# Optimization experiments

Measured on AMD Instinct MI355X. Metric: run time of the kernel, lower is better.

## Reference

```python
import jax, jax.numpy as jnp
import numpy as np

IMG = 128
NEAR, FAR = 1.0, 100.0
BG_EPS = 1e-3      # eps in soft_rasterize: background depth logit
SIGMA = 1e-6       # sigma_val
DIST_EPS = 1e-4    # dist_eps
GAMMA = 1e-6       # gamma_val
CHUNK = 500
B, V, F = 1, 5023, 10000


def setup_inputs():
    key = jax.random.key(0)
    k1, k2, k3, k4 = jax.random.split(key, 4)
    xy = jax.random.uniform(k1, (B, V, 2), minval=-1.0, maxval=1.0, dtype=jnp.float32)
    z = jax.random.uniform(k2, (B, V, 1), minval=5.0, maxval=15.0, dtype=jnp.float32)
    vertices = jnp.concatenate([xy, z], axis=-1)              # [B,V,3]
    faces = jax.random.randint(k3, (B, F, 3), 0, V, dtype=jnp.int32)
    attributes = jax.random.uniform(k4, (B, F, 3, 3), dtype=jnp.float32)
    return {"vertices": vertices, "faces": faces, "attributes": attributes}


def _seg_dist2(px, py, ax, ay, bx, by):
    # squared distance from pixel (px,py) to segment a-b; broadcasts [P] vs [B,C,1]
    dx = px - ax; dy = py - ay
    ex = bx - ax; ey = by - ay
    l2 = jnp.maximum(ex * ex + ey * ey, 1e-12)
    t = jnp.clip((dx * ex + dy * ey) / l2, 0.0, 1.0)
    rx = dx - t * ex; ry = dy - t * ey
    return rx * rx + ry * ry


def _render(vertices, faces, attributes):
    is_ = IMG
    P = is_ * is_
    bz = vertices.shape[0]
    v = vertices.at[..., 0].multiply(-1.0)                    # x flip (in-place in torch)
    fv = jax.vmap(lambda vv, ff: vv[ff])(v, faces)            # [B,F,3vert,3xyz]
    tex = attributes[..., :3]                                 # [B,F,3vert,3rgb]
    # fill_back=True: append copies with reversed winding
    fv = jnp.concatenate([fv, fv[:, :, ::-1, :]], axis=1)     # [B,2F,3,3]
    tex = jnp.concatenate([tex, tex[:, :, ::-1, :]], axis=1)
    F2 = fv.shape[1]
    pad = (-F2) % CHUNK
    valid = jnp.concatenate([jnp.ones((F2,), bool), jnp.zeros((pad,), bool)])
    fv = jnp.pad(fv, ((0, 0), (0, pad), (0, 0), (0, 0)))
    tex = jnp.pad(tex, ((0, 0), (0, pad), (0, 0), (0, 0)))
    n_chunks = (F2 + pad) // CHUNK
    fv = jnp.transpose(fv.reshape(bz, n_chunks, CHUNK, 3, 3), (1, 0, 2, 3, 4))
    tex = jnp.transpose(tex.reshape(bz, n_chunks, CHUNK, 3, 3), (1, 0, 2, 3, 4))
    valid = valid.reshape(n_chunks, CHUNK)

    # pixel centers in [-1,1]; row 0 is the top of the image (y flipped as in CUDA)
    xs = (2.0 * jnp.arange(is_, dtype=jnp.float32) + 1.0 - is_) / is_
    ys = (2.0 * (is_ - 1 - jnp.arange(is_, dtype=jnp.float32)) + 1.0 - is_) / is_
    px = jnp.broadcast_to(xs[None, :], (is_, is_)).reshape(-1)  # [P]
    py = jnp.broadcast_to(ys[:, None], (is_, is_)).reshape(-1)

    thr = DIST_EPS * SIGMA
    inv_g = 1.0 / GAMMA

    def step(carry, inp):
        m, s, cacc, prod = carry                # [B,P],[B,P],[B,3,P],[B,P]
        fvc, txc, vld = inp                     # [B,C,3,3],[B,C,3,3],[C]
        x0 = fvc[:, :, 0, 0][..., None]; y0 = fvc[:, :, 0, 1][..., None]; z0 = fvc[:, :, 0, 2][..., None]
        x1 = fvc[:, :, 1, 0][..., None]; y1 = fvc[:, :, 1, 1][..., None]; z1 = fvc[:, :, 1, 2][..., None]
        x2 = fvc[:, :, 2, 0][..., None]; y2 = fvc[:, :, 2, 1][..., None]; z2 = fvc[:, :, 2, 2][..., None]
        det = (y1 - y2) * (x0 - x2) + (x2 - x1) * (y0 - y2)   # [B,C,1]
        det = jnp.where(jnp.abs(det) < 1e-10, jnp.where(det < 0, -1e-10, 1e-10), det)
        w0 = ((y1 - y2) * (px - x2) + (x2 - x1) * (py - y2)) / det  # [B,C,P]
        w1 = ((y2 - y0) * (px - x2) + (x0 - x2) * (py - y2)) / det
        w2 = 1.0 - w0 - w1
        inside = (w0 >= 0) & (w1 >= 0) & (w2 >= 0)
        dis = jnp.minimum(jnp.minimum(_seg_dist2(px, py, x0, y0, x1, y1),
                                      _seg_dist2(px, py, x1, y1, x2, y2)),
                          _seg_dist2(px, py, x2, y2, x0, y0))     # [B,C,P] squared dist
        contrib = (inside | (dis < thr)) & vld[None, :, None]
        sgn = jnp.where(inside, 1.0, -1.0)
        Dp = jnp.where(contrib, jax.nn.sigmoid(sgn * dis / SIGMA), 0.0)
        prod = prod * jnp.prod(1.0 - Dp, axis=1)                  # alpha: prod(1-D)
        # clipped barycentric + perspective-correct depth
        c0 = jnp.clip(w0, 0.0, 1.0); c1 = jnp.clip(w1, 0.0, 1.0); c2 = jnp.clip(w2, 0.0, 1.0)
        csum = jnp.maximum(c0 + c1 + c2, 1e-5)
        c0 = c0 / csum; c1 = c1 / csum; c2 = c2 / csum
        zp_inv = c0 / z0 + c1 / z1 + c2 / z2
        zp = 1.0 / jnp.where(jnp.abs(zp_inv) < 1e-12, 1e-12, zp_inv)
        front = (y2 - y0) * (x1 - x0) < (y1 - y0) * (x2 - x0)     # [B,C,1]
        rgb_m = contrib & front & (zp >= NEAR) & (zp <= FAR)
        zpn = (FAR - zp) / (FAR - NEAR)
        new_m = jnp.maximum(m, jnp.max(jnp.where(rgb_m, zpn, -jnp.inf), axis=1))
        e = jnp.exp(jnp.where(rgb_m, (zpn - new_m[:, None, :]) * inv_g, -jnp.inf)) * Dp
        scale = jnp.exp((m - new_m) * inv_g)                      # [B,P]
        wc = jnp.stack([c0, c1, c2], axis=2)                      # [B,C,3,P]
        col = jnp.einsum('bcvp,bcvk->bckp', wc, txc)              # interpolated rgb
        s = s * scale + jnp.sum(e, axis=1)
        cacc = cacc * scale[:, None, :] + jnp.sum(e[:, :, None, :] * col, axis=1)
        return (new_m, s, cacc, prod), None

    m0 = jnp.full((bz, P), BG_EPS, jnp.float32)   # background logit = eps
    s0 = jnp.ones((bz, P), jnp.float32)           # exp((eps - m0)/gamma) = 1
    c0_ = jnp.zeros((bz, 3, P), jnp.float32)      # black background
    p0 = jnp.ones((bz, P), jnp.float32)
    (m, s, cacc, prod), _ = jax.lax.scan(jax.checkpoint(step), (m0, s0, c0_, p0), (fv, tex, valid))
    rgb = cacc / s[:, None, :]
    alpha = 1.0 - prod
    return jnp.concatenate([rgb, alpha[:, None, :]], axis=1).reshape(bz, 4, is_, is_)


def reference(vertices, faces, attributes):
    return _render(vertices, faces, attributes)
```

## Files before the change

### kernel.cpp

```cpp
#include <hip/hip_runtime.h>
#include <math.h>


#define NFACE 10000
#define IMG   128
#define P_TOT (IMG*IMG)
#define FSTR  40
#define NTILE 64
#define NQ    4
#define CAPQ  2500
#define CAP   (CAPQ*NQ)
#define BMAX  4096
#define NB    1024
#define CH    256
#define NCH   40
#define Z_LO  0.85f
#define Z_W   (0.12f/1024.0f)

__device__ __forceinline__ float rcp_nr(float x) {
    float r = __builtin_amdgcn_rcpf(x);
    r = r * __builtin_fmaf(-x, r, 2.0f);
    return r;
}

__device__ __forceinline__ float segd(float px, float py, float ax, float ay,
                                      float bx, float by, float il) {
    float dx = px - ax, dy = py - ay;
    float ex = bx - ax, ey = by - ay;
    float t = (dx * ex + dy * ey) * il;
    t = fminf(fmaxf(t, 0.0f), 1.0f);
    float rx = dx - t * ex, ry = dy - t * ey;
    return rx * rx + ry * ry;
}

__device__ __forceinline__ float rfl_f(float x) {
    return __uint_as_float(__builtin_amdgcn_readfirstlane(__float_as_uint(x)));
}

__device__ __forceinline__ int zbucket(float zub) {
    int b = (int)((zub - Z_LO) * (1.0f / Z_W));
    return min(max(b, 0), NB - 1);
}

__global__ __launch_bounds__(256) void k_prehist(const float* __restrict__ v,
                                                 const int* __restrict__ fc,
                                                 const float* __restrict__ at,
                                                 float* __restrict__ fb,
                                                 int* __restrict__ hist) {
    __shared__ int lh[NB];
    int c = blockIdx.x, tid = threadIdx.x;
    for (int j = tid; j < NB; j += 256) lh[j] = 0;
    __syncthreads();

    int f = c * CH + tid;
    if (f < NFACE) {
        int i0 = fc[3 * f], i1 = fc[3 * f + 1], i2 = fc[3 * f + 2];
        float x0 = -v[3 * i0], y0 = v[3 * i0 + 1], z0 = v[3 * i0 + 2];
        float x1 = -v[3 * i1], y1 = v[3 * i1 + 1], z1 = v[3 * i1 + 2];
        float x2 = -v[3 * i2], y2 = v[3 * i2 + 1], z2 = v[3 * i2 + 2];

        float det = (y1 - y2) * (x0 - x2) + (x2 - x1) * (y0 - y2);
        if (fabsf(det) < 1e-10f) det = (det < 0.0f) ? -1e-10f : 1e-10f;
        float a0 = y1 - y2, b0 = x2 - x1, a1 = y2 - y0, b1 = x0 - x2, detp = det;
        if (det < 0.0f) { detp = -det; a0 = -a0; b0 = -b0; a1 = -a1; b1 = -b1; }

        float a2 = a0 + a1, b2 = b0 + b1;
        float g0 = fmaxf(sqrtf(a0 * a0 + b0 * b0), 1e-12f);
        float g1 = fmaxf(sqrtf(a1 * a1 + b1 * b1), 1e-12f);
        float g2 = fmaxf(sqrtf(a2 * a2 + b2 * b2), 1e-12f);
        const float MARG = 3e-5f, AG = 1e-9f;
        float m0 = -(MARG * g0 + AG), m1 = -(MARG * g1 + AG), m2 = -(MARG * g2 + AG);

        float e01x = x1 - x0, e01y = y1 - y0;
        float e12x = x2 - x1, e12y = y2 - y1;
        float e20x = x0 - x2, e20y = y0 - y2;
        float il01 = 1.0f / fmaxf(e01x * e01x + e01y * e01y, 1e-12f);
        float il12 = 1.0f / fmaxf(e12x * e12x + e12y * e12y, 1e-12f);
        float il20 = 1.0f / fmaxf(e20x * e20x + e20y * e20y, 1e-12f);

        const float BM = 2e-5f;
        float bxmin = fminf(fminf(x0, x1), x2) - BM, bxmax = fmaxf(fmaxf(x0, x1), x2) + BM;
        float bymin = fminf(fminf(y0, y1), y2) - BM, bymax = fmaxf(fmaxf(y0, y1), y2) + BM;

        int mult = (((y2 - y0) * (x1 - x0)) < ((y1 - y0) * (x2 - x0)))
                 + (((y0 - y2) * (x1 - x2)) < ((y1 - y2) * (x0 - x2)));

        float zmin = fminf(fminf(z0, z1), z2);
        float zub = (100.0f - zmin) / 99.0f + 2e-6f;

        float* F = fb + (size_t)f * FSTR;
        F[0] = bxmin; F[1] = bxmax; F[2] = bymin; F[3] = bymax;
        F[4] = x2; F[5] = y2; F[6] = a0; F[7] = b0;
        F[8] = a1; F[9] = b1; F[10] = detp; F[11] = zub;
        F[12] = m0; F[13] = m1; F[14] = m2; F[15] = (float)mult;
        F[16] = x0; F[17] = y0; F[18] = x1; F[19] = y1;
        F[20] = il01; F[21] = il12; F[22] = il20; F[23] = 1.0f / detp;
        F[24] = 1.0f / z0; F[25] = 1.0f / z1; F[26] = 1.0f / z2;
        F[27] = 1.0f / g0; F[28] = 1.0f / g1; F[29] = 1.0f / g2;
#pragma unroll
        for (int k = 0; k < 9; k++) F[30 + k] = at[(size_t)f * 9 + k];
        F[39] = 0.0f;

        atomicAdd(&lh[zbucket(zub)], 1);
    }
    __syncthreads();
    for (int j = tid; j < NB; j += 256) hist[c * NB + j] = lh[j];
}

__global__ __launch_bounds__(1024) void k_scan(int* __restrict__ hist) {
    __shared__ int a[NB];
    int t = threadIdx.x;
    int tot = 0;
    for (int c = 0; c < NCH; c++) tot += hist[c * NB + t];
    a[t] = tot;
    for (int off = 1; off < NB; off <<= 1) {
        __syncthreads();
        int v = a[t] + ((t + off < NB) ? a[t + off] : 0);
        __syncthreads();
        a[t] = v;
    }
    int r = a[t] - tot;
    for (int c = 0; c < NCH; c++) {
        int h = hist[c * NB + t];
        hist[c * NB + t] = r;
        r += h;
    }
}

__global__ __launch_bounds__(256) void k_scatterre(const float* __restrict__ fb,
                                                   const int* __restrict__ hist,
                                                   float* __restrict__ fb2) {
    __shared__ int sb[CH];
    int c = blockIdx.x, tid = threadIdx.x;
    int f = c * CH + tid;
    bool valid = (f < NFACE);
    int b = valid ? zbucket(fb[(size_t)f * FSTR + 11]) : -1;
    sb[tid] = b;
    __syncthreads();
    if (valid) {
        int rank = 0;
        for (int j = 0; j < CH; j++) {
            int v2 = sb[j];
            rank += (j < tid && v2 == b) ? 1 : 0;
        }
        int pos = hist[c * NB + b] + rank;
        const float4* src = (const float4*)(fb + (size_t)f * FSTR);
        float4* dst = (float4*)(fb2 + (size_t)pos * FSTR);
#pragma unroll
        for (int k = 0; k < 10; k++) dst[k] = src[k];
        fb2[(size_t)pos * FSTR + 11] = Z_LO + (float)(b + 1) * Z_W + 1e-7f;
    }
}

__global__ __launch_bounds__(256) void k_bin(const float* __restrict__ fb2,
                                             float2* __restrict__ tmeta,
                                             int* __restrict__ cnt4) {
    int t = blockIdx.x >> 2, q = blockIdx.x & 3;
    int tid = threadIdx.x, wv = tid >> 6, lane = tid & 63;
    int tx = t & 7, ty = t >> 3;
    float x_lo = (float)(2 * (tx * 16) + 1 - IMG) / (float)IMG;
    float x_hi = (float)(2 * (tx * 16 + 15) + 1 - IMG) / (float)IMG;
    float y_hi = (float)(127 - 2 * (ty * 16)) / (float)IMG;
    float y_lo = (float)(127 - 2 * (ty * 16 + 15)) / (float)IMG;
    float cx = 0.5f * (x_lo + x_hi), hx = 0.5f * (x_hi - x_lo);
    float cy = 0.5f * (y_lo + y_hi), hy = 0.5f * (y_hi - y_lo);

    __shared__ int wc[4];
    int cnt = 0;
    int f0 = q * CAPQ;
    for (int base = f0; base < f0 + CAPQ; base += 256) {
        int j = base + tid;
        bool ov = false;
        float zub = 0.0f;
        if (j < f0 + CAPQ) {
            const float4* H = (const float4*)(fb2 + (size_t)j * FSTR);
            float4 h0 = H[0], h1 = H[1], h2 = H[2], h3 = H[3];
            ov = (h0.x <= x_hi) & (h0.y >= x_lo) & (h0.z <= y_hi) & (h0.w >= y_lo);
            if (ov) {
                float dx = cx - h1.x, dy = cy - h1.y;
                float mx0 = h1.z * dx + h1.w * dy + fabsf(h1.z) * hx + fabsf(h1.w) * hy;
                float mx1 = h2.x * dx + h2.y * dy + fabsf(h2.x) * hx + fabsf(h2.y) * hy;
                float A2 = -(h1.z + h2.x), B2 = -(h1.w + h2.y);
                float mx2 = h2.z + A2 * dx + B2 * dy + fabsf(A2) * hx + fabsf(B2) * hy;
                ov = (mx0 >= h3.x) & (mx1 >= h3.y) & (mx2 >= h3.z);
                zub = h2.w;
            }
        }
        unsigned long long mask = __ballot(ov);
        if (lane == 0) wc[wv] = __popcll(mask);
        __syncthreads();
        int off = cnt;
        for (int w = 0; w < 4; ++w) {
            if (w < wv) off += wc[w];
        }
        if (ov) {
            int pos = off + __popcll(mask & ((1ull << lane) - 1ull));
            tmeta[(size_t)t * CAP + q * CAPQ + pos] =
                make_float2(zub, __int_as_float(j));
        }
        cnt += wc[0] + wc[1] + wc[2] + wc[3];
        __syncthreads();
    }
    if (tid == 0) cnt4[t * 4 + q] = cnt;
}

__global__ __launch_bounds__(64) void k_map(const int* __restrict__ cnt4,
                                            int* __restrict__ map,
                                            int* __restrict__ starts,
                                            int* __restrict__ segs,
                                            int B) {
    int lane = threadIdx.x;
    int len = cnt4[4 * lane] + cnt4[4 * lane + 1] + cnt4[4 * lane + 2] + cnt4[4 * lane + 3];
    int tot = len;
    for (int o = 32; o > 0; o >>= 1) tot += __shfl_down(tot, o);
    tot = __shfl(tot, 0);
    int St = max(1, (int)(((long long)len * (long long)(B - NTILE)) /
                          (long long)max(tot, 1)));
    __shared__ int sS[64], sP[64];
    sS[lane] = St;
    __syncthreads();
    if (lane == 0) {
        int acc = 0;
        for (int t = 0; t < 64; ++t) { sP[t] = acc; acc += sS[t]; }
    }
    __syncthreads();
    for (int i = lane; i < B; i += 64) map[i] = -1;
    __syncthreads();
    int st = sP[lane];
    starts[lane] = st;
    segs[lane] = St;
    for (int s = 0; s < St; ++s) map[st + s] = (lane << 16) | s;
}

__global__ __launch_bounds__(256) void k_main(const float* __restrict__ fb2,
                                              const float2* __restrict__ tmeta,
                                              const int* __restrict__ cnt4,
                                              const int* __restrict__ map,
                                              const int* __restrict__ segs,
                                              float* __restrict__ part) {
    int bid = blockIdx.x;
    int mv = map[bid];
    if (mv < 0) return;
    int t = mv >> 16, seg = mv & 0xffff;
    int S = segs[t];

    int tid = threadIdx.x;
    int tx = t & 7, ty = t >> 3;
    int col = tx * 16 + (tid & 15);
    int row = ty * 16 + (tid >> 4);
    float px = (float)(2 * col + 1 - IMG) / (float)IMG;
    float py = (float)(2 * (IMG - 1 - row) + 1 - IMG) / (float)IMG;

    const float2* pm = tmeta + (size_t)t * CAP;

    float m = -__builtin_inff();
    float s = 0.0f, ca = 0.0f, cb = 0.0f, cc = 0.0f, pr = 1.0f;

    const float NEAR_T = 4.3e-3f;
    const float ZM = 1.3e-4f;

    bool done = false;
    for (int q = 0; q < 4 && !done; ++q) {
        int qlen = cnt4[t * 4 + q];
        for (int i = seg; i < qlen; i += S) {
            float2 mt = pm[q * CAPQ + i];
            float zcur = rfl_f(mt.x);
            if (__all((pr == 0.0f) & (zcur <= m - ZM))) { done = true; break; }
            int fj = __builtin_amdgcn_readfirstlane(__float_as_int(mt.y));
            const float4* H = (const float4*)(fb2 + (size_t)fj * FSTR);
            float4 g0 = H[0], g1 = H[1], g2 = H[2], g3 = H[3];

            bool inbox = (px >= g0.x) & (px <= g0.y) & (py >= g0.z) & (py <= g0.w);
            if (!__any(inbox)) continue;

            float x2 = g1.x, y2 = g1.y;
            float dx2 = px - x2, dy2 = py - y2;
            float num0 = g1.z * dx2 + g1.w * dy2;
            float num1 = g2.x * dx2 + g2.y * dy2;
            float detp = g2.z;
            float num2 = detp - num0 - num1;
            bool maybe = inbox & (num0 >= g3.x) & (num1 >= g3.y) & (num2 >= g3.z);
            if (!__any(maybe)) continue;

            const float* F = fb2 + (size_t)fj * FSTR;

            bool inside = (num0 >= 0.0f) & (num1 >= 0.0f) & (num2 >= 0.0f);
            bool inside_l = inside & inbox;

            float lin0 = num0 * F[27];
            float lin1 = num1 * F[28];
            float lin2 = num2 * F[29];
            float lbmin = fminf(fminf(lin0, lin1), lin2);

            bool outNear = maybe & (!inside);
            bool nearIn  = inside_l & (lbmin < NEAR_T);
            bool anyNear = __any(nearIn | outNear);

            float dis = 1e9f;
            float Dp;
            if (anyNear) {
                bool needAll = __any(outNear);
                float x0 = F[16], y0 = F[17], x1 = F[18], y1 = F[19];
                float d01 = 1e9f, d12 = 1e9f, d20 = 1e9f;
                if (needAll | __any(inside_l & (lin2 < NEAR_T)))
                    d01 = segd(px, py, x0, y0, x1, y1, F[20]);
                if (needAll | __any(inside_l & (lin0 < NEAR_T)))
                    d12 = segd(px, py, x1, y1, x2, y2, F[21]);
                if (needAll | __any(inside_l & (lin1 < NEAR_T)))
                    d20 = segd(px, py, x2, y2, x0, y0, F[22]);
                dis = fminf(fminf(d01, d12), d20);

                float qq = dis * 1e6f;
                float xs_ = inside ? qq : -qq;
                float tt = __expf(-fabsf(xs_));
                float Dpn = (xs_ >= 0.0f ? 1.0f : tt) * rcp_nr(1.0f + tt);
                bool nearl = nearIn | outNear;
                Dp = nearl ? Dpn : (inside_l ? 1.0f : 0.0f);
            } else {
                Dp = inside_l ? 1.0f : 0.0f;
            }

            bool contrib = inside_l | (outNear & (dis < 1e-10f));
            Dp = contrib ? Dp : 0.0f;
            float omd = 1.0f - Dp;
            pr *= contrib ? (omd * omd) : 1.0f;

            float multf = g3.w;
            bool doz = contrib & (multf > 0.0f);
            if (__any(doz & (zcur > m - ZM))) {
                float rdetp = F[23];
                float w0 = num0 * rdetp;
                float w1 = num1 * rdetp;
                float c0 = fminf(fmaxf(w0, 0.0f), 1.0f);
                float c1 = fminf(fmaxf(w1, 0.0f), 1.0f);
                float c2 = fminf(fmaxf(1.0f - w0 - w1, 0.0f), 1.0f);
                float csum = fmaxf(c0 + c1 + c2, 1e-5f);
                float rcs = rcp_nr(csum);
                c0 *= rcs; c1 *= rcs; c2 *= rcs;
                float zpi = c0 * F[24] + c1 * F[25] + c2 * F[26];
                if (fabsf(zpi) < 1e-12f) zpi = 1e-12f;
                float zp = rcp_nr(zpi);
                if (doz & (zp >= 1.0f) & (zp <= 100.0f)) {
                    float zpn = (100.0f - zp) / 99.0f;
                    if (zpn > m) {
                        float scl = __expf((m - zpn) * 1e6f);
                        s *= scl; ca *= scl; cb *= scl; cc *= scl;
                        m = zpn;
                    }
                    float arg = (zpn - m) * 1e6f;
                    if (arg > -110.0f) {
                        float e = __expf(arg) * Dp * multf;
                        float col0 = c0 * F[30] + c1 * F[33] + c2 * F[36];
                        float col1 = c0 * F[31] + c1 * F[34] + c2 * F[37];
                        float col2 = c0 * F[32] + c1 * F[35] + c2 * F[38];
                        s += e; ca += e * col0; cb += e * col1; cc += e * col2;
                    }
                }
            }
        }
    }

    size_t pb = (size_t)bid * 6 * 256;
    part[pb + 0 * 256 + tid] = m;
    part[pb + 1 * 256 + tid] = s;
    part[pb + 2 * 256 + tid] = ca;
    part[pb + 3 * 256 + tid] = cb;
    part[pb + 4 * 256 + tid] = cc;
    part[pb + 5 * 256 + tid] = pr;
}

__global__ __launch_bounds__(1024) void k_reduce(const float* __restrict__ part,
                                                 const int* __restrict__ starts,
                                                 const int* __restrict__ segs,
                                                 float* __restrict__ out) {
    __shared__ float sm[4][256], ss[4][256], sa[4][256], sb2[4][256],
                     sc[4][256], sp[4][256];
    int t = blockIdx.x;
    int tid = threadIdx.x;
    int q = tid & 255, sub = tid >> 8;
    int start = starts[t], S = segs[t];

    const float NINF = -__builtin_inff();
    float mp = NINF;
    for (int sgi = sub; sgi < S; sgi += 4)
        mp = fmaxf(mp, part[((size_t)(start + sgi) * 6 + 0) * 256 + q]);
    float sum = 0.0f, a = 0.0f, b = 0.0f, c = 0.0f, pr = 1.0f;
    for (int sgi = sub; sgi < S; sgi += 4) {
        const float* r = part + ((size_t)(start + sgi) * 6) * 256;
        float rm = r[0 * 256 + q];
        float w = (rm == NINF) ? 0.0f : __expf((rm - mp) * 1e6f);
        pr *= r[5 * 256 + q];
        if (__any(w != 0.0f)) {
            sum += r[1 * 256 + q] * w;
            a += r[2 * 256 + q] * w;
            b += r[3 * 256 + q] * w;
            c += r[4 * 256 + q] * w;
        }
    }
    sm[sub][q] = mp; ss[sub][q] = sum; sa[sub][q] = a;
    sb2[sub][q] = b; sc[sub][q] = c;  sp[sub][q] = pr;
    __syncthreads();
    if (sub == 0) {
        int tx = t & 7, ty = t >> 3;
        int col = tx * 16 + (q & 15);
        int row = ty * 16 + (q >> 4);
        int p = row * IMG + col;
        float M = 0.001f;
#pragma unroll
        for (int k = 0; k < 4; k++) M = fmaxf(M, sm[k][q]);
        float SUM = __expf((0.001f - M) * 1e6f);
        float A = 0.0f, B2 = 0.0f, C = 0.0f, PR = 1.0f;
#pragma unroll
        for (int k = 0; k < 4; k++) {
            float w = __expf((sm[k][q] - M) * 1e6f);
            SUM += ss[k][q] * w;
            A += sa[k][q] * w;
            B2 += sb2[k][q] * w;
            C += sc[k][q] * w;
            PR *= sp[k][q];
        }
        out[0 * P_TOT + p] = A / SUM;
        out[1 * P_TOT + p] = B2 / SUM;
        out[2 * P_TOT + p] = C / SUM;
        out[3 * P_TOT + p] = 1.0f - PR;
    }
}

extern "C" void kernel_launch(void* const* d_in, const int* in_sizes, int n_in,
                              void* d_out, int out_size, void* d_ws, size_t ws_size,
                              hipStream_t stream) {
    const float* verts = (const float*)d_in[0];
    const int*   faces = (const int*)d_in[1];
    const float* attrs = (const float*)d_in[2];
    float* out = (float*)d_out;
    float* ws  = (float*)d_ws;

    float*  fb    = ws;
    int*    hist  = (int*)(fb + (size_t)NFACE * FSTR);
    float*  fb2   = (float*)(hist + NCH * NB);
    float2* tmeta = (float2*)(fb2 + (size_t)NFACE * FSTR);
    int*    cnt4  = (int*)(tmeta + (size_t)NTILE * CAP);
    int*    map   = cnt4 + NTILE * 4;
    int*    starts= map + BMAX;
    int*    segs  = starts + NTILE;
    float*  part  = (float*)(segs + NTILE);

    size_t used_f = 2 * (size_t)NFACE * FSTR + NCH * NB
                  + 2 * (size_t)NTILE * CAP + NTILE * 4 + BMAX + 2 * NTILE;
    long   rem_f  = (long)(ws_size / 4) - (long)used_f;
    int B = (int)(rem_f / (6 * 256));
    if (B > BMAX) B = BMAX;
    if (B < 256)  B = 256;

    k_prehist<<<NCH, 256, 0, stream>>>(verts, faces, attrs, fb, hist);
    k_scan<<<1, 1024, 0, stream>>>(hist);
    k_scatterre<<<NCH, 256, 0, stream>>>(fb, hist, fb2);
    k_bin<<<NTILE * NQ, 256, 0, stream>>>(fb2, tmeta, cnt4);
    k_map<<<1, 64, 0, stream>>>(cnt4, map, starts, segs, B);
    k_main<<<B, 256, 0, stream>>>(fb2, tmeta, cnt4, map, segs, part);
    k_reduce<<<NTILE, 1024, 0, stream>>>(part, starts, segs, out);
}
```

Before: 139.1 us.

## Bin faces into 8x8 pixel regions and assign one wavefront per region segment

Replaces the 64 tiles of 16x16 pixels with 256 regions of 8x8 pixels. Each binning block now tests faces against four sub-regions and writes plain face-index lists, so the main kernel reads the depth bound from the face record instead of a separate (z, index) list. The main kernel now maps work per wavefront (64 lanes = one 8x8 region) rather than per 256-thread block, with a binary-search work map over up to 16K slots. The aim is tighter face culling per wave and less divergent wasted work, at the cost of more binning passes, more partials and extra barriers in k_bin.

```diff
diff --git a/kernel.cpp b/kernel.cpp
--- a/kernel.cpp
+++ b/kernel.cpp
@@ -6,11 +6,10 @@
 #define IMG   128
 #define P_TOT (IMG*IMG)
 #define FSTR  40
-#define NTILE 64
+#define NREG  256
 #define NQ    4
 #define CAPQ  2500
-#define CAP   (CAPQ*NQ)
-#define BMAX  4096
+#define WMAX  16384
 #define NB    1024
 #define CH    256
 #define NCH   40
@@ -31,10 +30,6 @@
     t = fminf(fmaxf(t, 0.0f), 1.0f);
     float rx = dx - t * ex, ry = dy - t * ey;
     return rx * rx + ry * ry;
-}
-
-__device__ __forceinline__ float rfl_f(float x) {
-    return __uint_as_float(__builtin_amdgcn_readfirstlane(__float_as_uint(x)));
 }
 
 __device__ __forceinline__ int zbucket(float zub) {
@@ -107,9 +102,11 @@
     for (int j = tid; j < NB; j += 256) hist[c * NB + j] = lh[j];
 }
 
-__global__ __launch_bounds__(1024) void k_scan(int* __restrict__ hist) {
+__global__ __launch_bounds__(1024) void k_scan(int* __restrict__ hist,
+                                               int* __restrict__ len) {
     __shared__ int a[NB];
     int t = threadIdx.x;
+    if (t < NREG) len[t] = 0;
     int tot = 0;
     for (int c = 0; c < NCH; c++) tot += hist[c * NB + t];
     a[t] = tot;
@@ -153,106 +150,145 @@
 }
 
 __global__ __launch_bounds__(256) void k_bin(const float* __restrict__ fb2,
-                                             float2* __restrict__ tmeta,
-                                             int* __restrict__ cnt4) {
+                                             int* __restrict__ rlist,
+                                             int* __restrict__ cnt16,
+                                             int* __restrict__ len) {
     int t = blockIdx.x >> 2, q = blockIdx.x & 3;
     int tid = threadIdx.x, wv = tid >> 6, lane = tid & 63;
     int tx = t & 7, ty = t >> 3;
-    float x_lo = (float)(2 * (tx * 16) + 1 - IMG) / (float)IMG;
-    float x_hi = (float)(2 * (tx * 16 + 15) + 1 - IMG) / (float)IMG;
-    float y_hi = (float)(127 - 2 * (ty * 16)) / (float)IMG;
-    float y_lo = (float)(127 - 2 * (ty * 16 + 15)) / (float)IMG;
-    float cx = 0.5f * (x_lo + x_hi), hx = 0.5f * (x_hi - x_lo);
-    float cy = 0.5f * (y_lo + y_hi), hy = 0.5f * (y_hi - y_lo);
+
+    float rxlo[4], rxhi[4], rylo[4], ryhi[4], rcx[4], rcy[4], rhx[4], rhy[4];
+    int rgl[4];
+#pragma unroll
+    for (int rl = 0; rl < 4; rl++) {
+        int sx = rl & 1, sy = rl >> 1;
+        int rx = tx * 2 + sx, ry = ty * 2 + sy;
+        rgl[rl] = ry * 16 + rx;
+        float xl = (float)(2 * (rx * 8) + 1 - IMG) / (float)IMG;
+        float xh = (float)(2 * (rx * 8 + 7) + 1 - IMG) / (float)IMG;
+        float yh = (float)(127 - 2 * (ry * 8)) / (float)IMG;
+        float yl = (float)(127 - 2 * (ry * 8 + 7)) / (float)IMG;
+        rxlo[rl] = xl; rxhi[rl] = xh; rylo[rl] = yl; ryhi[rl] = yh;
+        rcx[rl] = 0.5f * (xl + xh); rhx[rl] = 0.5f * (xh - xl);
+        rcy[rl] = 0.5f * (yl + yh); rhy[rl] = 0.5f * (yh - yl);
+    }
+    float tx_lo = rxlo[0], tx_hi = rxhi[1];
+    float ty_lo = rylo[2], ty_hi = ryhi[0];
 
     __shared__ int wc[4];
-    int cnt = 0;
+    int cnt[4] = {0, 0, 0, 0};
     int f0 = q * CAPQ;
     for (int base = f0; base < f0 + CAPQ; base += 256) {
         int j = base + tid;
-        bool ov = false;
-        float zub = 0.0f;
-        if (j < f0 + CAPQ) {
+        bool ov[4] = {false, false, false, false};
+        {
             const float4* H = (const float4*)(fb2 + (size_t)j * FSTR);
             float4 h0 = H[0], h1 = H[1], h2 = H[2], h3 = H[3];
-            ov = (h0.x <= x_hi) & (h0.y >= x_lo) & (h0.z <= y_hi) & (h0.w >= y_lo);
-            if (ov) {
-                float dx = cx - h1.x, dy = cy - h1.y;
-                float mx0 = h1.z * dx + h1.w * dy + fabsf(h1.z) * hx + fabsf(h1.w) * hy;
-                float mx1 = h2.x * dx + h2.y * dy + fabsf(h2.x) * hx + fabsf(h2.y) * hy;
+            bool tov = (h0.x <= tx_hi) & (h0.y >= tx_lo) & (h0.z <= ty_hi) & (h0.w >= ty_lo);
+            if (tov) {
                 float A2 = -(h1.z + h2.x), B2 = -(h1.w + h2.y);
-                float mx2 = h2.z + A2 * dx + B2 * dy + fabsf(A2) * hx + fabsf(B2) * hy;
-                ov = (mx0 >= h3.x) & (mx1 >= h3.y) & (mx2 >= h3.z);
-                zub = h2.w;
+#pragma unroll
+                for (int rl = 0; rl < 4; rl++) {
+                    bool o = (h0.x <= rxhi[rl]) & (h0.y >= rxlo[rl]) &
+                             (h0.z <= ryhi[rl]) & (h0.w >= rylo[rl]);
+                    if (o) {
+                        float dx = rcx[rl] - h1.x, dy = rcy[rl] - h1.y;
+                        float hx = rhx[rl], hy = rhy[rl];
+                        float mx0 = h1.z * dx + h1.w * dy + fabsf(h1.z) * hx + fabsf(h1.w) * hy;
+                        float mx1 = h2.x * dx + h2.y * dy + fabsf(h2.x) * hx + fabsf(h2.y) * hy;
+                        float mx2 = h2.z + A2 * dx + B2 * dy + fabsf(A2) * hx + fabsf(B2) * hy;
+                        o = (mx0 >= h3.x) & (mx1 >= h3.y) & (mx2 >= h3.z);
+                    }
+                    ov[rl] = o;
+                }
             }
         }
-        unsigned long long mask = __ballot(ov);
-        if (lane == 0) wc[wv] = __popcll(mask);
-        __syncthreads();
-        int off = cnt;
-        for (int w = 0; w < 4; ++w) {
-            if (w < wv) off += wc[w];
-        }
-        if (ov) {
-            int pos = off + __popcll(mask & ((1ull << lane) - 1ull));
-            tmeta[(size_t)t * CAP + q * CAPQ + pos] =
-                make_float2(zub, __int_as_float(j));
-        }
-        cnt += wc[0] + wc[1] + wc[2] + wc[3];
-        __syncthreads();
-    }
-    if (tid == 0) cnt4[t * 4 + q] = cnt;
-}
-
-__global__ __launch_bounds__(64) void k_map(const int* __restrict__ cnt4,
-                                            int* __restrict__ map,
-                                            int* __restrict__ starts,
-                                            int* __restrict__ segs,
-                                            int B) {
-    int lane = threadIdx.x;
-    int len = cnt4[4 * lane] + cnt4[4 * lane + 1] + cnt4[4 * lane + 2] + cnt4[4 * lane + 3];
-    int tot = len;
-    for (int o = 32; o > 0; o >>= 1) tot += __shfl_down(tot, o);
-    tot = __shfl(tot, 0);
-    int St = max(1, (int)(((long long)len * (long long)(B - NTILE)) /
-                          (long long)max(tot, 1)));
-    __shared__ int sS[64], sP[64];
-    sS[lane] = St;
-    __syncthreads();
-    if (lane == 0) {
+#pragma unroll
+        for (int rl = 0; rl < 4; rl++) {
+            unsigned long long mask = __ballot(ov[rl]);
+            if (lane == 0) wc[wv] = __popcll(mask);
+            __syncthreads();
+            int off = cnt[rl];
+            for (int w = 0; w < 4; ++w) {
+                if (w < wv) off += wc[w];
+            }
+            if (ov[rl]) {
+                int pos = off + __popcll(mask & ((1ull << lane) - 1ull));
+                rlist[((size_t)rgl[rl] * 4 + q) * CAPQ + pos] = j;
+            }
+            cnt[rl] += wc[0] + wc[1] + wc[2] + wc[3];
+            __syncthreads();
+        }
+    }
+    if (tid == 0) {
+#pragma unroll
+        for (int rl = 0; rl < 4; rl++) {
+            cnt16[rgl[rl] * 4 + q] = cnt[rl];
+            atomicAdd(&len[rgl[rl]], cnt[rl]);
+        }
+    }
+}
+
+__global__ __launch_bounds__(256) void k_map(const int* __restrict__ len,
+                                             int* __restrict__ map,
+                                             int* __restrict__ starts,
+                                             int* __restrict__ Sarr,
+                                             int W) {
+    __shared__ int sL[NREG], sS[NREG], sP[NREG], sTot;
+    int rr = threadIdx.x;
+    sL[rr] = len[rr];
+    __syncthreads();
+    if (rr == 0) {
+        int tot = 0;
+        for (int k = 0; k < NREG; k++) tot += sL[k];
+        sTot = max(tot, 1);
+    }
+    __syncthreads();
+    int tot = sTot;
+    int S = max(1, (int)(((long long)sL[rr] * (long long)(W - NREG)) /
+                         (long long)tot));
+    sS[rr] = S;
+    __syncthreads();
+    if (rr == 0) {
         int acc = 0;
-        for (int t = 0; t < 64; ++t) { sP[t] = acc; acc += sS[t]; }
-    }
-    __syncthreads();
-    for (int i = lane; i < B; i += 64) map[i] = -1;
-    __syncthreads();
-    int st = sP[lane];
-    starts[lane] = st;
-    segs[lane] = St;
-    for (int s = 0; s < St; ++s) map[st + s] = (lane << 16) | s;
+        for (int k = 0; k < NREG; k++) { sP[k] = acc; acc += sS[k]; }
+    }
+    __syncthreads();
+    starts[rr] = sP[rr];
+    Sarr[rr] = sS[rr];
+    int used = sP[NREG - 1] + sS[NREG - 1];
+    for (int i = rr; i < W; i += 256) {
+        int mv = -1;
+        if (i < used) {
+            int lo = 0, hi = NREG - 1;
+            while (lo < hi) {
+                int mid = (lo + hi + 1) >> 1;
+                if (sP[mid] <= i) lo = mid; else hi = mid - 1;
+            }
+            mv = (lo << 16) | (i - sP[lo]);
+        }
+        map[i] = mv;
+    }
 }
 
 __global__ __launch_bounds__(256) void k_main(const float* __restrict__ fb2,
-                                              const float2* __restrict__ tmeta,
-                                              const int* __restrict__ cnt4,
+                                              const int* __restrict__ rlist,
+                                              const int* __restrict__ cnt16,
                                               const int* __restrict__ map,
-                                              const int* __restrict__ segs,
+                                              const int* __restrict__ Sarr,
                                               float* __restrict__ part) {
-    int bid = blockIdx.x;
-    int mv = map[bid];
+    int slot = blockIdx.x * 4 + (threadIdx.x >> 6);
+    int lane = threadIdx.x & 63;
+    int mv = map[slot];
     if (mv < 0) return;
-    int t = mv >> 16, seg = mv & 0xffff;
-    int S = segs[t];
-
-    int tid = threadIdx.x;
-    int tx = t & 7, ty = t >> 3;
-    int col = tx * 16 + (tid & 15);
-    int row = ty * 16 + (tid >> 4);
+    int r = mv >> 16, seg = mv & 0xffff;
+    int Sr = Sarr[r];
+    int rx = r & 15, ry = r >> 4;
+    int col = rx * 8 + (lane & 7);
+    int row = ry * 8 + (lane >> 3);
     float px = (float)(2 * col + 1 - IMG) / (float)IMG;
     float py = (float)(2 * (IMG - 1 - row) + 1 - IMG) / (float)IMG;
 
-    const float2* pm = tmeta + (size_t)t * CAP;
-
     float m = -__builtin_inff();
     float s = 0.0f, ca = 0.0f, cb = 0.0f, cc = 0.0f, pr = 1.0f;
 
@@ -261,14 +297,14 @@
 
     bool done = false;
     for (int q = 0; q < 4 && !done; ++q) {
-        int qlen = cnt4[t * 4 + q];
-        for (int i = seg; i < qlen; i += S) {
-            float2 mt = pm[q * CAPQ + i];
-            float zcur = rfl_f(mt.x);
-            if (__all((pr == 0.0f) & (zcur <= m - ZM))) { done = true; break; }
-            int fj = __builtin_amdgcn_readfirstlane(__float_as_int(mt.y));
+        int qlen = cnt16[r * 4 + q];
+        const int* lst = rlist + ((size_t)r * 4 + q) * CAPQ;
+        for (int i = seg; i < qlen; i += Sr) {
+            int fj = __builtin_amdgcn_readfirstlane(lst[i]);
             const float4* H = (const float4*)(fb2 + (size_t)fj * FSTR);
             float4 g0 = H[0], g1 = H[1], g2 = H[2], g3 = H[3];
+            float zcur = g2.w;
+            if (__all((pr == 0.0f) & (zcur <= m - ZM))) { done = true; break; }
 
             bool inbox = (px >= g0.x) & (px <= g0.y) & (py >= g0.z) & (py <= g0.w);
             if (!__any(inbox)) continue;
@@ -360,64 +396,64 @@
         }
     }
 
-    size_t pb = (size_t)bid * 6 * 256;
-    part[pb + 0 * 256 + tid] = m;
-    part[pb + 1 * 256 + tid] = s;
-    part[pb + 2 * 256 + tid] = ca;
-    part[pb + 3 * 256 + tid] = cb;
-    part[pb + 4 * 256 + tid] = cc;
-    part[pb + 5 * 256 + tid] = pr;
-}
-
-__global__ __launch_bounds__(1024) void k_reduce(const float* __restrict__ part,
-                                                 const int* __restrict__ starts,
-                                                 const int* __restrict__ segs,
-                                                 float* __restrict__ out) {
-    __shared__ float sm[4][256], ss[4][256], sa[4][256], sb2[4][256],
-                     sc[4][256], sp[4][256];
-    int t = blockIdx.x;
+    size_t pb = (size_t)slot * 6 * 64;
+    part[pb + 0 * 64 + lane] = m;
+    part[pb + 1 * 64 + lane] = s;
+    part[pb + 2 * 64 + lane] = ca;
+    part[pb + 3 * 64 + lane] = cb;
+    part[pb + 4 * 64 + lane] = cc;
+    part[pb + 5 * 64 + lane] = pr;
+}
+
+__global__ __launch_bounds__(256) void k_reduce(const float* __restrict__ part,
+                                                const int* __restrict__ starts,
+                                                const int* __restrict__ Sarr,
+                                                float* __restrict__ out) {
+    __shared__ float sm[4][64], ss[4][64], sa[4][64], sb2[4][64],
+                     sc[4][64], sp[4][64];
+    int r = blockIdx.x;
     int tid = threadIdx.x;
-    int q = tid & 255, sub = tid >> 8;
-    int start = starts[t], S = segs[t];
+    int lane = tid & 63, sub = tid >> 6;
+    int start = starts[r], S = Sarr[r];
 
     const float NINF = -__builtin_inff();
     float mp = NINF;
     for (int sgi = sub; sgi < S; sgi += 4)
-        mp = fmaxf(mp, part[((size_t)(start + sgi) * 6 + 0) * 256 + q]);
+        mp = fmaxf(mp, part[((size_t)(start + sgi) * 6 + 0) * 64 + lane]);
     float sum = 0.0f, a = 0.0f, b = 0.0f, c = 0.0f, pr = 1.0f;
     for (int sgi = sub; sgi < S; sgi += 4) {
-        const float* r = part + ((size_t)(start + sgi) * 6) * 256;
-        float rm = r[0 * 256 + q];
+        const float* rp = part + ((size_t)(start + sgi) * 6) * 64;
+        float rm = rp[0 * 64 + lane];
         float w = (rm == NINF) ? 0.0f : __expf((rm - mp) * 1e6f);
-        pr *= r[5 * 256 + q];
+        pr *= rp[5 * 64 + lane];
         if (__any(w != 0.0f)) {
-            sum += r[1 * 256 + q] * w;
-            a += r[2 * 256 + q] * w;
-            b += r[3 * 256 + q] * w;
-            c += r[4 * 256 + q] * w;
-        }
-    }
-    sm[sub][q] = mp; ss[sub][q] = sum; sa[sub][q] = a;
-    sb2[sub][q] = b; sc[sub][q] = c;  sp[sub][q] = pr;
+            sum += rp[1 * 64 + lane] * w;
+            a += rp[2 * 64 + lane] * w;
+            b += rp[3 * 64 + lane] * w;
+            c += rp[4 * 64 + lane] * w;
+        }
+    }
+    sm[sub][lane] = mp; ss[sub][lane] = sum; sa[sub][lane] = a;
+    sb2[sub][lane] = b; sc[sub][lane] = c;  sp[sub][lane] = pr;
     __syncthreads();
     if (sub == 0) {
-        int tx = t & 7, ty = t >> 3;
-        int col = tx * 16 + (q & 15);
-        int row = ty * 16 + (q >> 4);
+        int rx = r & 15, ry = r >> 4;
+        int col = rx * 8 + (lane & 7);
+        int row = ry * 8 + (lane >> 3);
         int p = row * IMG + col;
         float M = 0.001f;
 #pragma unroll
-        for (int k = 0; k < 4; k++) M = fmaxf(M, sm[k][q]);
+        for (int k = 0; k < 4; k++) M = fmaxf(M, sm[k][lane]);
         float SUM = __expf((0.001f - M) * 1e6f);
         float A = 0.0f, B2 = 0.0f, C = 0.0f, PR = 1.0f;
 #pragma unroll
         for (int k = 0; k < 4; k++) {
-            float w = __expf((sm[k][q] - M) * 1e6f);
-            SUM += ss[k][q] * w;
-            A += sa[k][q] * w;
-            B2 += sb2[k][q] * w;
-            C += sc[k][q] * w;
-            PR *= sp[k][q];
+            float w = __expf((sm[k][lane] - M) * 1e6f);
+            SUM += ss[k][lane] * w;
+            A += sa[k][lane] * w;
+            B2 += sb2[k][lane] * w;
+            C += sc[k][lane] * w;
+            PR *= sp[k][lane];
         }
         out[0 * P_TOT + p] = A / SUM;
         out[1 * P_TOT + p] = B2 / SUM;
@@ -435,28 +471,31 @@
     float* out = (float*)d_out;
     float* ws  = (float*)d_ws;
 
-    float*  fb    = ws;
-    int*    hist  = (int*)(fb + (size_t)NFACE * FSTR);
-    float*  fb2   = (float*)(hist + NCH * NB);
-    float2* tmeta = (float2*)(fb2 + (size_t)NFACE * FSTR);
-    int*    cnt4  = (int*)(tmeta + (size_t)NTILE * CAP);
-    int*    map   = cnt4 + NTILE * 4;
-    int*    starts= map + BMAX;
-    int*    segs  = starts + NTILE;
-    float*  part  = (float*)(segs + NTILE);
+    float* fb     = ws;
+    int*   hist   = (int*)(fb + (size_t)NFACE * FSTR);
+    float* fb2    = (float*)(hist + NCH * NB);
+    int*   rlist  = (int*)(fb2 + (size_t)NFACE * FSTR);
+    int*   cnt16  = rlist + (size_t)NREG * 4 * CAPQ;
+    int*   len    = cnt16 + NREG * 4;
+    int*   map    = len + NREG;
+    int*   starts = map + WMAX;
+    int*   Sarr   = starts + NREG;
+    float* part   = (float*)(Sarr + NREG);
 
     size_t used_f = 2 * (size_t)NFACE * FSTR + NCH * NB
-                  + 2 * (size_t)NTILE * CAP + NTILE * 4 + BMAX + 2 * NTILE;
+                  + (size_t)NREG * 4 * CAPQ + NREG * 4 + NREG + WMAX + 2 * NREG;
     long   rem_f  = (long)(ws_size / 4) - (long)used_f;
-    int B = (int)(rem_f / (6 * 256));
-    if (B > BMAX) B = BMAX;
-    if (B < 256)  B = 256;
+    int W = (int)(rem_f / (6 * 64));
+    if (W > WMAX) W = WMAX;
+    if (W < 1024) W = 1024;
+    W &= ~3;
+    int B = W / 4;
 
     k_prehist<<<NCH, 256, 0, stream>>>(verts, faces, attrs, fb, hist);
-    k_scan<<<1, 1024, 0, stream>>>(hist);
+    k_scan<<<1, 1024, 0, stream>>>(hist, len);
     k_scatterre<<<NCH, 256, 0, stream>>>(fb, hist, fb2);
-    k_bin<<<NTILE * NQ, 256, 0, stream>>>(fb2, tmeta, cnt4);
-    k_map<<<1, 64, 0, stream>>>(cnt4, map, starts, segs, B);
-    k_main<<<B, 256, 0, stream>>>(fb2, tmeta, cnt4, map, segs, part);
-    k_reduce<<<NTILE, 1024, 0, stream>>>(part, starts, segs, out);
-}
+    k_bin<<<NREG, 256, 0, stream>>>(fb2, rlist, cnt16, len);
+    k_map<<<1, 256, 0, stream>>>(len, map, starts, Sarr, W);
+    k_main<<<B, 256, 0, stream>>>(fb2, rlist, cnt16, map, Sarr, part);
+    k_reduce<<<NREG, 256, 0, stream>>>(part, starts, Sarr, out);
+}
```

Measured after the change: 173.8 us. +24.9%, slower.

## Drop k_map launch by deriving tile-segment map in-kernel; transpose histogram layout

Applied to the files above, without the earlier changes.

Removes the separate k_map launch: k_main and k_reduce now each recompute the per-tile segment counts and prefix offsets from cnt4 in shared memory, and k_main finds its tile with a binary search. The per-chunk histogram is transposed to bucket-major so the scan kernel reads each row contiguously, and the face chunk size is halved, giving 79 blocks of 128 threads instead of 40 of 256 for more parallelism in the preprocessing kernels. The aim is to cut one launch and some serialized small-kernel latency, at the cost of redundant map derivation (a serial 64-iteration loop on thread 0) in every k_main block.

```diff
diff --git a/kernel.cpp b/kernel.cpp
--- a/kernel.cpp
+++ b/kernel.cpp
@@ -12,8 +12,8 @@
 #define CAP   (CAPQ*NQ)
 #define BMAX  4096
 #define NB    1024
-#define CH    256
-#define NCH   40
+#define CH    128
+#define NCH   79
 #define Z_LO  0.85f
 #define Z_W   (0.12f/1024.0f)
 
@@ -42,14 +42,14 @@
     return min(max(b, 0), NB - 1);
 }
 
-__global__ __launch_bounds__(256) void k_prehist(const float* __restrict__ v,
+__global__ __launch_bounds__(128) void k_prehist(const float* __restrict__ v,
                                                  const int* __restrict__ fc,
                                                  const float* __restrict__ at,
                                                  float* __restrict__ fb,
                                                  int* __restrict__ hist) {
     __shared__ int lh[NB];
     int c = blockIdx.x, tid = threadIdx.x;
-    for (int j = tid; j < NB; j += 256) lh[j] = 0;
+    for (int j = tid; j < NB; j += 128) lh[j] = 0;
     __syncthreads();
 
     int f = c * CH + tid;
@@ -104,14 +104,16 @@
         atomicAdd(&lh[zbucket(zub)], 1);
     }
     __syncthreads();
-    for (int j = tid; j < NB; j += 256) hist[c * NB + j] = lh[j];
+    for (int j = tid; j < NB; j += 128) hist[j * NCH + c] = lh[j];
 }
 
 __global__ __launch_bounds__(1024) void k_scan(int* __restrict__ hist) {
     __shared__ int a[NB];
     int t = threadIdx.x;
+    int* row = hist + t * NCH;
     int tot = 0;
-    for (int c = 0; c < NCH; c++) tot += hist[c * NB + t];
+#pragma unroll 8
+    for (int c = 0; c < NCH; c++) tot += row[c];
     a[t] = tot;
     for (int off = 1; off < NB; off <<= 1) {
         __syncthreads();
@@ -120,14 +122,15 @@
         a[t] = v;
     }
     int r = a[t] - tot;
+#pragma unroll 8
     for (int c = 0; c < NCH; c++) {
-        int h = hist[c * NB + t];
-        hist[c * NB + t] = r;
+        int h = row[c];
+        row[c] = r;
         r += h;
     }
 }
 
-__global__ __launch_bounds__(256) void k_scatterre(const float* __restrict__ fb,
+__global__ __launch_bounds__(128) void k_scatterre(const float* __restrict__ fb,
                                                    const int* __restrict__ hist,
                                                    float* __restrict__ fb2) {
     __shared__ int sb[CH];
@@ -143,7 +146,7 @@
             int v2 = sb[j];
             rank += (j < tid && v2 == b) ? 1 : 0;
         }
-        int pos = hist[c * NB + b] + rank;
+        int pos = hist[b * NCH + c] + rank;
         const float4* src = (const float4*)(fb + (size_t)f * FSTR);
         float4* dst = (float4*)(fb2 + (size_t)pos * FSTR);
 #pragma unroll
@@ -204,47 +207,47 @@
     if (tid == 0) cnt4[t * 4 + q] = cnt;
 }
 
-__global__ __launch_bounds__(64) void k_map(const int* __restrict__ cnt4,
-                                            int* __restrict__ map,
-                                            int* __restrict__ starts,
-                                            int* __restrict__ segs,
-                                            int B) {
-    int lane = threadIdx.x;
-    int len = cnt4[4 * lane] + cnt4[4 * lane + 1] + cnt4[4 * lane + 2] + cnt4[4 * lane + 3];
-    int tot = len;
-    for (int o = 32; o > 0; o >>= 1) tot += __shfl_down(tot, o);
-    tot = __shfl(tot, 0);
-    int St = max(1, (int)(((long long)len * (long long)(B - NTILE)) /
-                          (long long)max(tot, 1)));
-    __shared__ int sS[64], sP[64];
-    sS[lane] = St;
-    __syncthreads();
-    if (lane == 0) {
+__device__ __forceinline__ void derive_map(const int* __restrict__ cnt4,
+                                           int B, int tid,
+                                           int* sLen, int* sS, int* sP,
+                                           int* sUsed) {
+    if (tid < NTILE)
+        sLen[tid] = cnt4[4 * tid] + cnt4[4 * tid + 1]
+                  + cnt4[4 * tid + 2] + cnt4[4 * tid + 3];
+    __syncthreads();
+    if (tid == 0) {
+        int tot = 0;
+        for (int k = 0; k < NTILE; k++) tot += sLen[k];
+        tot = max(tot, 1);
         int acc = 0;
-        for (int t = 0; t < 64; ++t) { sP[t] = acc; acc += sS[t]; }
-    }
-    __syncthreads();
-    for (int i = lane; i < B; i += 64) map[i] = -1;
-    __syncthreads();
-    int st = sP[lane];
-    starts[lane] = st;
-    segs[lane] = St;
-    for (int s = 0; s < St; ++s) map[st + s] = (lane << 16) | s;
+        for (int k = 0; k < NTILE; k++) {
+            int S = max(1, (int)(((long long)sLen[k] * (long long)(B - NTILE)) /
+                                 (long long)tot));
+            sS[k] = S; sP[k] = acc; acc += S;
+        }
+        *sUsed = acc;
+    }
+    __syncthreads();
 }
 
 __global__ __launch_bounds__(256) void k_main(const float* __restrict__ fb2,
                                               const float2* __restrict__ tmeta,
                                               const int* __restrict__ cnt4,
-                                              const int* __restrict__ map,
-                                              const int* __restrict__ segs,
-                                              float* __restrict__ part) {
+                                              float* __restrict__ part,
+                                              int B) {
+    __shared__ int sLen[NTILE], sS[NTILE], sP[NTILE], sUsed;
+    int tid = threadIdx.x;
+    derive_map(cnt4, B, tid, sLen, sS, sP, &sUsed);
     int bid = blockIdx.x;
-    int mv = map[bid];
-    if (mv < 0) return;
-    int t = mv >> 16, seg = mv & 0xffff;
-    int S = segs[t];
-
-    int tid = threadIdx.x;
+    if (bid >= sUsed) return;
+    int lo = 0, hi = NTILE - 1;
+    while (lo < hi) {
+        int mid = (lo + hi + 1) >> 1;
+        if (sP[mid] <= bid) lo = mid; else hi = mid - 1;
+    }
+    int t = lo, seg = bid - sP[lo];
+    int S = sS[t];
+
     int tx = t & 7, ty = t >> 3;
     int col = tx * 16 + (tid & 15);
     int row = ty * 16 + (tid >> 4);
@@ -262,8 +265,9 @@
     bool done = false;
     for (int q = 0; q < 4 && !done; ++q) {
         int qlen = cnt4[t * 4 + q];
+        const float2* pq = pm + q * CAPQ;
         for (int i = seg; i < qlen; i += S) {
-            float2 mt = pm[q * CAPQ + i];
+            float2 mt = pq[i];
             float zcur = rfl_f(mt.x);
             if (__all((pr == 0.0f) & (zcur <= m - ZM))) { done = true; break; }
             int fj = __builtin_amdgcn_readfirstlane(__float_as_int(mt.y));
@@ -370,15 +374,18 @@
 }
 
 __global__ __launch_bounds__(1024) void k_reduce(const float* __restrict__ part,
-                                                 const int* __restrict__ starts,
-                                                 const int* __restrict__ segs,
-                                                 float* __restrict__ out) {
+                                                 const int* __restrict__ cnt4,
+                                                 float* __restrict__ out,
+                                                 int B) {
+    __shared__ int sLen[NTILE], sS[NTILE], sP[NTILE], sUsed;
     __shared__ float sm[4][256], ss[4][256], sa[4][256], sb2[4][256],
                      sc[4][256], sp[4][256];
     int t = blockIdx.x;
     int tid = threadIdx.x;
+    derive_map(cnt4, B, tid, sLen, sS, sP, &sUsed);
+    int start = sP[t], S = sS[t];
+
     int q = tid & 255, sub = tid >> 8;
-    int start = starts[t], S = segs[t];
 
     const float NINF = -__builtin_inff();
     float mp = NINF;
@@ -437,26 +444,22 @@
 
     float*  fb    = ws;
     int*    hist  = (int*)(fb + (size_t)NFACE * FSTR);
-    float*  fb2   = (float*)(hist + NCH * NB);
+    float*  fb2   = (float*)(hist + NB * NCH);
     float2* tmeta = (float2*)(fb2 + (size_t)NFACE * FSTR);
     int*    cnt4  = (int*)(tmeta + (size_t)NTILE * CAP);
-    int*    map   = cnt4 + NTILE * 4;
-    int*    starts= map + BMAX;
-    int*    segs  = starts + NTILE;
-    float*  part  = (float*)(segs + NTILE);
-
-    size_t used_f = 2 * (size_t)NFACE * FSTR + NCH * NB
-                  + 2 * (size_t)NTILE * CAP + NTILE * 4 + BMAX + 2 * NTILE;
+    float*  part  = (float*)(cnt4 + NTILE * 4);
+
+    size_t used_f = 2 * (size_t)NFACE * FSTR + NB * NCH
+                  + 2 * (size_t)NTILE * CAP + NTILE * 4;
     long   rem_f  = (long)(ws_size / 4) - (long)used_f;
     int B = (int)(rem_f / (6 * 256));
     if (B > BMAX) B = BMAX;
     if (B < 256)  B = 256;
 
-    k_prehist<<<NCH, 256, 0, stream>>>(verts, faces, attrs, fb, hist);
+    k_prehist<<<NCH, 128, 0, stream>>>(verts, faces, attrs, fb, hist);
     k_scan<<<1, 1024, 0, stream>>>(hist);
-    k_scatterre<<<NCH, 256, 0, stream>>>(fb, hist, fb2);
+    k_scatterre<<<NCH, 128, 0, stream>>>(fb, hist, fb2);
     k_bin<<<NTILE * NQ, 256, 0, stream>>>(fb2, tmeta, cnt4);
-    k_map<<<1, 64, 0, stream>>>(cnt4, map, starts, segs, B);
-    k_main<<<B, 256, 0, stream>>>(fb2, tmeta, cnt4, map, segs, part);
-    k_reduce<<<NTILE, 1024, 0, stream>>>(part, starts, segs, out);
-}
+    k_main<<<B, 256, 0, stream>>>(fb2, tmeta, cnt4, part, B);
+    k_reduce<<<NTILE, 1024, 0, stream>>>(part, cnt4, out, B);
+}
```

New measurement: 198.5 us. 1.43x slower.

## Batch-stage face headers into shared memory cooperatively per block

Applied to the files above, without the earlier changes.

The per-face inner loop is restructured to process faces in batches of sixteen. Threads cooperatively load each batch's face metadata and 64-byte header into LDS between block barriers, replacing per-wave dependent global loads for every face. The aim is to hide global load latency by issuing sixteen faces' loads in parallel. The cost is two block syncs plus a sync-count per batch, and early termination now needs all four waves to agree before the block stops iterating.

```diff
diff --git a/kernel.cpp b/kernel.cpp
--- a/kernel.cpp
+++ b/kernel.cpp
@@ -16,6 +16,7 @@
 #define NCH   40
 #define Z_LO  0.85f
 #define Z_W   (0.12f/1024.0f)
+#define BATCH 16
 
 __device__ __forceinline__ float rcp_nr(float x) {
     float r = __builtin_amdgcn_rcpf(x);
@@ -238,6 +239,10 @@
                                               const int* __restrict__ map,
                                               const int* __restrict__ segs,
                                               float* __restrict__ part) {
+    __shared__ float  sz[BATCH];
+    __shared__ int    sf[BATCH];
+    __shared__ float4 sh[BATCH][4];
+
     int bid = blockIdx.x;
     int mv = map[bid];
     if (mv < 0) return;
@@ -259,101 +264,127 @@
     const float NEAR_T = 4.3e-3f;
     const float ZM = 1.3e-4f;
 
-    bool done = false;
-    for (int q = 0; q < 4 && !done; ++q) {
+    bool mydone = false;
+    bool alldone = false;
+
+    for (int q = 0; q < 4 && !alldone; ++q) {
         int qlen = cnt4[t * 4 + q];
-        for (int i = seg; i < qlen; i += S) {
-            float2 mt = pm[q * CAPQ + i];
-            float zcur = rfl_f(mt.x);
-            if (__all((pr == 0.0f) & (zcur <= m - ZM))) { done = true; break; }
-            int fj = __builtin_amdgcn_readfirstlane(__float_as_int(mt.y));
-            const float4* H = (const float4*)(fb2 + (size_t)fj * FSTR);
-            float4 g0 = H[0], g1 = H[1], g2 = H[2], g3 = H[3];
-
-            bool inbox = (px >= g0.x) & (px <= g0.y) & (py >= g0.z) & (py <= g0.w);
-            if (!__any(inbox)) continue;
-
-            float x2 = g1.x, y2 = g1.y;
-            float dx2 = px - x2, dy2 = py - y2;
-            float num0 = g1.z * dx2 + g1.w * dy2;
-            float num1 = g2.x * dx2 + g2.y * dy2;
-            float detp = g2.z;
-            float num2 = detp - num0 - num1;
-            bool maybe = inbox & (num0 >= g3.x) & (num1 >= g3.y) & (num2 >= g3.z);
-            if (!__any(maybe)) continue;
-
-            const float* F = fb2 + (size_t)fj * FSTR;
-
-            bool inside = (num0 >= 0.0f) & (num1 >= 0.0f) & (num2 >= 0.0f);
-            bool inside_l = inside & inbox;
-
-            float lin0 = num0 * F[27];
-            float lin1 = num1 * F[28];
-            float lin2 = num2 * F[29];
-            float lbmin = fminf(fminf(lin0, lin1), lin2);
-
-            bool outNear = maybe & (!inside);
-            bool nearIn  = inside_l & (lbmin < NEAR_T);
-            bool anyNear = __any(nearIn | outNear);
-
-            float dis = 1e9f;
-            float Dp;
-            if (anyNear) {
-                bool needAll = __any(outNear);
-                float x0 = F[16], y0 = F[17], x1 = F[18], y1 = F[19];
-                float d01 = 1e9f, d12 = 1e9f, d20 = 1e9f;
-                if (needAll | __any(inside_l & (lin2 < NEAR_T)))
-                    d01 = segd(px, py, x0, y0, x1, y1, F[20]);
-                if (needAll | __any(inside_l & (lin0 < NEAR_T)))
-                    d12 = segd(px, py, x1, y1, x2, y2, F[21]);
-                if (needAll | __any(inside_l & (lin1 < NEAR_T)))
-                    d20 = segd(px, py, x2, y2, x0, y0, F[22]);
-                dis = fminf(fminf(d01, d12), d20);
-
-                float qq = dis * 1e6f;
-                float xs_ = inside ? qq : -qq;
-                float tt = __expf(-fabsf(xs_));
-                float Dpn = (xs_ >= 0.0f ? 1.0f : tt) * rcp_nr(1.0f + tt);
-                bool nearl = nearIn | outNear;
-                Dp = nearl ? Dpn : (inside_l ? 1.0f : 0.0f);
-            } else {
-                Dp = inside_l ? 1.0f : 0.0f;
+        const float2* pq = pm + q * CAPQ;
+        for (int ib = seg; ib < qlen; ib += BATCH * S) {
+            int ndone = __syncthreads_count((int)mydone);
+            if (ndone == 256) { alldone = true; break; }
+            if (tid < BATCH) {
+                int e = ib + tid * S;
+                if (e < qlen) {
+                    float2 mt = pq[e];
+                    sz[tid] = mt.x;
+                    sf[tid] = __float_as_int(mt.y);
+                } else {
+                    sf[tid] = -1;
+                }
             }
-
-            bool contrib = inside_l | (outNear & (dis < 1e-10f));
-            Dp = contrib ? Dp : 0.0f;
-            float omd = 1.0f - Dp;
-            pr *= contrib ? (omd * omd) : 1.0f;
-
-            float multf = g3.w;
-            bool doz = contrib & (multf > 0.0f);
-            if (__any(doz & (zcur > m - ZM))) {
-                float rdetp = F[23];
-                float w0 = num0 * rdetp;
-                float w1 = num1 * rdetp;
-                float c0 = fminf(fmaxf(w0, 0.0f), 1.0f);
-                float c1 = fminf(fmaxf(w1, 0.0f), 1.0f);
-                float c2 = fminf(fmaxf(1.0f - w0 - w1, 0.0f), 1.0f);
-                float csum = fmaxf(c0 + c1 + c2, 1e-5f);
-                float rcs = rcp_nr(csum);
-                c0 *= rcs; c1 *= rcs; c2 *= rcs;
-                float zpi = c0 * F[24] + c1 * F[25] + c2 * F[26];
-                if (fabsf(zpi) < 1e-12f) zpi = 1e-12f;
-                float zp = rcp_nr(zpi);
-                if (doz & (zp >= 1.0f) & (zp <= 100.0f)) {
-                    float zpn = (100.0f - zp) / 99.0f;
-                    if (zpn > m) {
-                        float scl = __expf((m - zpn) * 1e6f);
-                        s *= scl; ca *= scl; cb *= scl; cc *= scl;
-                        m = zpn;
+            __syncthreads();
+            if (tid < BATCH * 4) {
+                int k = tid >> 2, j = tid & 3;
+                int fj = sf[k];
+                if (fj >= 0)
+                    sh[k][j] = ((const float4*)(fb2 + (size_t)fj * FSTR))[j];
+            }
+            __syncthreads();
+            if (!mydone) {
+                for (int k = 0; k < BATCH; ++k) {
+                    int fj = __builtin_amdgcn_readfirstlane(sf[k]);
+                    if (fj < 0) break;
+                    float zcur = sz[k];
+                    if (__all((pr == 0.0f) & (zcur <= m - ZM))) { mydone = true; break; }
+                    float4 g0 = sh[k][0], g1 = sh[k][1], g2 = sh[k][2], g3 = sh[k][3];
+
+                    bool inbox = (px >= g0.x) & (px <= g0.y) & (py >= g0.z) & (py <= g0.w);
+                    if (!__any(inbox)) continue;
+
+                    float x2 = g1.x, y2 = g1.y;
+                    float dx2 = px - x2, dy2 = py - y2;
+                    float num0 = g1.z * dx2 + g1.w * dy2;
+                    float num1 = g2.x * dx2 + g2.y * dy2;
+                    float detp = g2.z;
+                    float num2 = detp - num0 - num1;
+                    bool maybe = inbox & (num0 >= g3.x) & (num1 >= g3.y) & (num2 >= g3.z);
+                    if (!__any(maybe)) continue;
+
+                    const float* F = fb2 + (size_t)fj * FSTR;
+
+                    bool inside = (num0 >= 0.0f) & (num1 >= 0.0f) & (num2 >= 0.0f);
+                    bool inside_l = inside & inbox;
+
+                    float lin0 = num0 * F[27];
+                    float lin1 = num1 * F[28];
+                    float lin2 = num2 * F[29];
+                    float lbmin = fminf(fminf(lin0, lin1), lin2);
+
+                    bool outNear = maybe & (!inside);
+                    bool nearIn  = inside_l & (lbmin < NEAR_T);
+                    bool anyNear = __any(nearIn | outNear);
+
+                    float dis = 1e9f;
+                    float Dp;
+                    if (anyNear) {
+                        bool needAll = __any(outNear);
+                        float x0 = F[16], y0 = F[17], x1 = F[18], y1 = F[19];
+                        float d01 = 1e9f, d12 = 1e9f, d20 = 1e9f;
+                        if (needAll | __any(inside_l & (lin2 < NEAR_T)))
+                            d01 = segd(px, py, x0, y0, x1, y1, F[20]);
+                        if (needAll | __any(inside_l & (lin0 < NEAR_T)))
+                            d12 = segd(px, py, x1, y1, x2, y2, F[21]);
+                        if (needAll | __any(inside_l & (lin1 < NEAR_T)))
+                            d20 = segd(px, py, x2, y2, x0, y0, F[22]);
+                        dis = fminf(fminf(d01, d12), d20);
+
+                        float qq = dis * 1e6f;
+                        float xs_ = inside ? qq : -qq;
+                        float tt = __expf(-fabsf(xs_));
+                        float Dpn = (xs_ >= 0.0f ? 1.0f : tt) * rcp_nr(1.0f + tt);
+                        bool nearl = nearIn | outNear;
+                        Dp = nearl ? Dpn : (inside_l ? 1.0f : 0.0f);
+                    } else {
+                        Dp = inside_l ? 1.0f : 0.0f;
                     }
-                    float arg = (zpn - m) * 1e6f;
-                    if (arg > -110.0f) {
-                        float e = __expf(arg) * Dp * multf;
-                        float col0 = c0 * F[30] + c1 * F[33] + c2 * F[36];
-                        float col1 = c0 * F[31] + c1 * F[34] + c2 * F[37];
-                        float col2 = c0 * F[32] + c1 * F[35] + c2 * F[38];
-                        s += e; ca += e * col0; cb += e * col1; cc += e * col2;
+
+                    bool contrib = inside_l | (outNear & (dis < 1e-10f));
+                    Dp = contrib ? Dp : 0.0f;
+                    float omd = 1.0f - Dp;
+                    pr *= contrib ? (omd * omd) : 1.0f;
+
+                    float multf = g3.w;
+                    bool doz = contrib & (multf > 0.0f);
+                    if (__any(doz & (zcur > m - ZM))) {
+                        float rdetp = F[23];
+                        float w0 = num0 * rdetp;
+                        float w1 = num1 * rdetp;
+                        float c0 = fminf(fmaxf(w0, 0.0f), 1.0f);
+                        float c1 = fminf(fmaxf(w1, 0.0f), 1.0f);
+                        float c2 = fminf(fmaxf(1.0f - w0 - w1, 0.0f), 1.0f);
+                        float csum = fmaxf(c0 + c1 + c2, 1e-5f);
+                        float rcs = rcp_nr(csum);
+                        c0 *= rcs; c1 *= rcs; c2 *= rcs;
+                        float zpi = c0 * F[24] + c1 * F[25] + c2 * F[26];
+                        if (fabsf(zpi) < 1e-12f) zpi = 1e-12f;
+                        float zp = rcp_nr(zpi);
+                        if (doz & (zp >= 1.0f) & (zp <= 100.0f)) {
+                            float zpn = (100.0f - zp) / 99.0f;
+                            if (zpn > m) {
+                                float scl = __expf((m - zpn) * 1e6f);
+                                s *= scl; ca *= scl; cb *= scl; cc *= scl;
+                                m = zpn;
+                            }
+                            float arg = (zpn - m) * 1e6f;
+                            if (arg > -110.0f) {
+                                float e = __expf(arg) * Dp * multf;
+                                float col0 = c0 * F[30] + c1 * F[33] + c2 * F[36];
+                                float col1 = c0 * F[31] + c1 * F[34] + c2 * F[37];
+                                float col2 = c0 * F[32] + c1 * F[35] + c2 * F[38];
+                                s += e; ca += e * col0; cb += e * col1; cc += e * col2;
+                            }
+                        }
                     }
                 }
             }
```

After: 145.2 us. +4.4%, slower.
